# Kernel optimization log

Measured on AMD Instinct MI355X. Metric: run time of the kernel, lower is better.

The kernel has to match this reference:

```python
import jax, jax.numpy as jnp
import numpy as np


def setup_inputs() -> dict:
    key = jax.random.key(0)
    k1, k2, k3, k4 = jax.random.split(key, 4)
    B, D_vis, E, N = 512, 4096, 1024, 512
    vf = jax.random.normal(k1, (B, D_vis), dtype=jnp.float32)
    p_lfs = jax.random.normal(k2, (B, E), dtype=jnp.float32)
    n_lfs = jax.random.normal(k3, (N, E), dtype=jnp.float32)
    W = jax.random.normal(k4, (E, D_vis), dtype=jnp.float32) * (1.0 / np.sqrt(D_vis))
    b = jnp.zeros((E,), dtype=jnp.float32)
    return {"vf": vf, "p_lfs": p_lfs, "n_lfs": n_lfs, "W": W, "b": b}


def _partial_order_sim(hypers, hypos):
    # -||relu(hypers - hypos)||_2 along last dim
    act = jax.nn.relu(hypers - hypos)
    return -jnp.sqrt(jnp.sum(act * act, axis=-1))


def reference(vf, p_lfs, n_lfs, W, b):
    # vf: [B, D_vis], W: [E, D_vis] -> vf_emb: [B, E]
    vf_emb = jnp.einsum("bd,ed->be", vf, W) + b
    # positive scores: [B]
    p_scores = _partial_order_sim(p_lfs, vf_emb)
    # negative scores, batched over B: n_lfs [N,E] vs vf_emb [B,E] -> [B,N]
    n_scores = _partial_order_sim(n_lfs[None, :, :], vf_emb[:, None, :])
    # score_stack: [B, 1+N]
    return jnp.concatenate([p_scores[:, None], n_scores], axis=1)
```

## Files before the change

kernel.cpp:

```cpp
#include <hip/hip_runtime.h>
#include <hip/hip_bf16.h>

constexpr int B = 512;
constexpr int D = 4096;
constexpr int E = 1024;
constexpr int N = 512;
constexpr int KS = 8;
constexpr int KC = D / KS;
constexpr int NSTEP = KC / 32;
constexpr int ES = 8;
constexpr int EC = E / ES;
constexpr int DEPTH = 4;

typedef __attribute__((ext_vector_type(8))) short bf16x8;
typedef __attribute__((ext_vector_type(4))) float f32x4;
typedef float v2f __attribute__((ext_vector_type(2)));

typedef __attribute__((address_space(3))) void lds_void;
typedef const __attribute__((address_space(1))) void gbl_void;

__device__ __forceinline__ unsigned short f2bf(float f) {
    __hip_bfloat16 h = __float2bfloat16(f);
    return *reinterpret_cast<unsigned short*>(&h);
}

__global__ __launch_bounds__(256) void cvt_all(
    const float* __restrict__ vf, const float* __restrict__ W,
    unsigned short* __restrict__ vfB, unsigned short* __restrict__ WB)
{
    const int bid = blockIdx.x;
    const float* src;
    unsigned short* dst;
    int i;
    if (bid < 1024) { src = vf; dst = vfB; i = (bid * 256 + threadIdx.x) * 8; }
    else           { src = W;  dst = WB;  i = ((bid - 1024) * 256 + threadIdx.x) * 8; }
    float4 v0 = *(const float4*)(src + i);
    float4 v1 = *(const float4*)(src + i + 4);
    bf16x8 o;
    o[0] = (short)f2bf(v0.x); o[1] = (short)f2bf(v0.y);
    o[2] = (short)f2bf(v0.z); o[3] = (short)f2bf(v0.w);
    o[4] = (short)f2bf(v1.x); o[5] = (short)f2bf(v1.y);
    o[6] = (short)f2bf(v1.z); o[7] = (short)f2bf(v1.w);
    *(bf16x8*)(dst + i) = o;
}

__global__ __launch_bounds__(64) void gemm_lds(
    const unsigned short* __restrict__ vf,
    const unsigned short* __restrict__ W,
    float* __restrict__ part)
{
    __shared__ unsigned short sA[DEPTH][2048];
    __shared__ unsigned short sB[DEPTH][2048];

    const int L  = threadIdx.x;

    const int id = blockIdx.x + 16 * blockIdx.y + 128 * blockIdx.z;
    const int l  = (id & 7) * 128 + (id >> 3);
    const int ks = l >> 7;
    const int n0 = (l & 15) * 64;
    const int m0 = ((l >> 4) & 7) * 64;

    const int subrow = L >> 2;
    const int qstg = (L & 3) ^ ((L >> 2) & 3) ^ ((L >> 4) & 3);
    const int kbeg = ks * KC;
    const unsigned short* aSrc[4];
    const unsigned short* bSrc[4];
    #pragma unroll
    for (int c = 0; c < 4; ++c) {
        aSrc[c] = vf + (size_t)(m0 + c * 16 + subrow) * D + kbeg + qstg * 8;
        bSrc[c] = W  + (size_t)(n0 + c * 16 + subrow) * D + kbeg + qstg * 8;
    }

    const int r16 = L & 15;
    const int quad = L >> 4;
    const int swz = quad ^ (r16 & 3) ^ ((r16 >> 2) & 3);
    const int aoff = r16 * 64 + swz * 16;

    f32x4 acc[4][4] = {};

    auto issue = [&](int step, int buf) {
        const size_t koff = (size_t)step * 32;
        #pragma unroll
        for (int c = 0; c < 4; ++c) {
            __builtin_amdgcn_global_load_lds(
                (gbl_void*)(aSrc[c] + koff),
                (lds_void*)((char*)&sA[buf][0] + c * 1024), 16, 0, 0);
            __builtin_amdgcn_global_load_lds(
                (gbl_void*)(bSrc[c] + koff),
                (lds_void*)((char*)&sB[buf][0] + c * 1024), 16, 0, 0);
        }
    };

    issue(0, 0);
    issue(1, 1);
    issue(2, 2);
    issue(3, 3);

    #define GSTEP(S, WC, ISS)                                                  \
    {                                                                          \
        const int buf_ = (S) & 3;                                              \
        __builtin_amdgcn_s_waitcnt(WC);                                        \
        bf16x8 af[4], bg[4];                                                   \
        _Pragma("unroll")                                                      \
        for (int i = 0; i < 4; ++i)                                            \
            af[i] = *(const bf16x8*)((const char*)&sA[buf_][0] + i * 1024 + aoff); \
        _Pragma("unroll")                                                      \
        for (int j = 0; j < 4; ++j)                                            \
            bg[j] = *(const bf16x8*)((const char*)&sB[buf_][0] + j * 1024 + aoff); \
        _Pragma("unroll")                                                      \
        for (int i = 0; i < 4; ++i)                                            \
            _Pragma("unroll")                                                  \
            for (int j = 0; j < 4; ++j)                                        \
                acc[i][j] = __builtin_amdgcn_mfma_f32_16x16x32_bf16(           \
                    af[i], bg[j], acc[i][j], 0, 0, 0);                         \
        if (ISS) issue((S) + DEPTH, buf_);                                     \
    }

    #pragma unroll 1
    for (int s = 0; s < NSTEP - DEPTH; ++s)
        GSTEP(s, 0x4F78, true);
    GSTEP(NSTEP - 4, 0x4F78, false);
    GSTEP(NSTEP - 3, 0x4F70, false);
    GSTEP(NSTEP - 2, 0x0F78, false);
    GSTEP(NSTEP - 1, 0x0F70, false);
    #undef GSTEP

    float* po = part + (size_t)ks * B * E;
    #pragma unroll
    for (int j = 0; j < 4; ++j) {
        const int col = n0 + j * 16 + r16;
        #pragma unroll
        for (int i = 0; i < 4; ++i) {
            const int row = m0 + i * 16 + quad * 4;
            #pragma unroll
            for (int r = 0; r < 4; ++r)
                po[(size_t)(row + r) * E + col] = acc[i][j][r];
        }
    }
}

__global__ __launch_bounds__(256) void reduce_emb(
    const float* __restrict__ part, const float* __restrict__ bias,
    float* __restrict__ emb)
{
    const int idx = (blockIdx.x * 256 + threadIdx.x) * 4;
    const int col = idx & (E - 1);
    float4 s = *(const float4*)(bias + col);
    #pragma unroll
    for (int ks = 0; ks < KS; ++ks) {
        float4 p = *(const float4*)(part + (size_t)ks * B * E + idx);
        s.x += p.x; s.y += p.y; s.z += p.z; s.w += p.w;
    }
    *(float4*)(emb + idx) = s;
}

__global__ __launch_bounds__(256, 2) void scores_part(
    const float* __restrict__ emb,
    const float* __restrict__ n_lfs,
    float* __restrict__ pn)
{
    constexpr int LDW = EC + 2;
    __shared__ float eS[64 * LDW];
    __shared__ float nS[64 * LDW];

    const int t  = threadIdx.x;
    const int n0 = blockIdx.x * 64;
    const int b0 = blockIdx.y * 64;
    const int e0 = blockIdx.z * EC;

    {
        const int row = t >> 2;
        const int cb  = (t & 3) * 32;
        const float* ep = emb   + (size_t)(b0 + row) * E + e0 + cb;
        const float* np = n_lfs + (size_t)(n0 + row) * E + e0 + cb;
        float* ed = &eS[row * LDW + cb];
        float* nd = &nS[row * LDW + cb];
        #pragma unroll
        for (int q = 0; q < 8; ++q) {
            float4 v = *(const float4*)(ep + q * 4);
            float4 w = *(const float4*)(np + q * 4);
            *(v2f*)(ed + q * 4)     = (v2f){v.x, v.y};
            *(v2f*)(ed + q * 4 + 2) = (v2f){v.z, v.w};
            *(v2f*)(nd + q * 4)     = (v2f){w.x, w.y};
            *(v2f*)(nd + q * 4 + 2) = (v2f){w.z, w.w};
        }
    }
    __syncthreads();

    const int ty = t >> 4;
    const int tx = t & 15;

    const v2f z = {0.f, 0.f};
    v2f acc[4][4] = {{z,z,z,z},{z,z,z,z},{z,z,z,z},{z,z,z,z}};

    #pragma unroll 4
    for (int e = 0; e < EC; e += 2) {
        v2f a[4], c[4];
        #pragma unroll
        for (int r = 0; r < 4; ++r)
            a[r] = *(const v2f*)&eS[(ty + 16 * r) * LDW + e];
        #pragma unroll
        for (int q = 0; q < 4; ++q)
            c[q] = *(const v2f*)&nS[(tx + 16 * q) * LDW + e];
        #pragma unroll
        for (int r = 0; r < 4; ++r)
            #pragma unroll
            for (int q = 0; q < 4; ++q) {
                v2f d = c[q] - a[r];
                d = __builtin_elementwise_max(d, z);
                acc[r][q] = __builtin_elementwise_fma(d, d, acc[r][q]);
            }
    }

    float* po = pn + (size_t)blockIdx.z * B * N;
    #pragma unroll
    for (int r = 0; r < 4; ++r) {
        const size_t ob = (size_t)(b0 + ty + 16 * r) * N;
        #pragma unroll
        for (int q = 0; q < 4; ++q)
            po[ob + n0 + tx + 16 * q] = acc[r][q].x + acc[r][q].y;
    }
}

__global__ __launch_bounds__(256) void scores_final(
    const float* __restrict__ pn,
    const float* __restrict__ emb,
    const float* __restrict__ p_lfs,
    float* __restrict__ out)
{
    const int t = threadIdx.x;
    if (blockIdx.x < 1024) {
        const int i = blockIdx.x * 256 + t;
        const int b = i >> 9;
        const int n = i & (N - 1);
        float s = 0.f;
        #pragma unroll
        for (int z = 0; z < ES; ++z)
            s += pn[(size_t)z * B * N + i];
        out[(size_t)b * 513 + 1 + n] = -sqrtf(s);
        return;
    }
    const int b0 = (blockIdx.x - 1024) * 32;
    const int r = t >> 3;
    const int g = t & 7;
    const float* pr = p_lfs + (size_t)(b0 + r) * E;
    const float* er = emb   + (size_t)(b0 + r) * E;
    float acc = 0.f;
    for (int e = g * 4; e < E; e += 32) {
        float4 p = *(const float4*)(pr + e);
        float4 v = *(const float4*)(er + e);
        float d;
        d = p.x - v.x; d = fmaxf(d, 0.f); acc = fmaf(d, d, acc);
        d = p.y - v.y; d = fmaxf(d, 0.f); acc = fmaf(d, d, acc);
        d = p.z - v.z; d = fmaxf(d, 0.f); acc = fmaf(d, d, acc);
        d = p.w - v.w; d = fmaxf(d, 0.f); acc = fmaf(d, d, acc);
    }
    #pragma unroll
    for (int off = 4; off; off >>= 1) acc += __shfl_down(acc, off, 8);
    if (g == 0) out[(size_t)(b0 + r) * 513] = -sqrtf(acc);
}

extern "C" void kernel_launch(void* const* d_in, const int* in_sizes, int n_in,
                              void* d_out, int out_size, void* d_ws, size_t ws_size,
                              hipStream_t stream) {
    const float* vf    = (const float*)d_in[0];
    const float* p_lfs = (const float*)d_in[1];
    const float* n_lfs = (const float*)d_in[2];
    const float* W     = (const float*)d_in[3];
    const float* bias  = (const float*)d_in[4];
    float* out = (float*)d_out;

    char* ws = (char*)d_ws;
    float*          pg  = (float*)ws;
    float*          pn  = (float*)ws;
    unsigned short* vfB = (unsigned short*)(ws + ((size_t)16 << 20));
    unsigned short* WB  = (unsigned short*)(ws + ((size_t)20 << 20));
    float*          emb = (float*)(ws + ((size_t)28 << 20));

    cvt_all<<<3072, 256, 0, stream>>>(vf, W, vfB, WB);

    dim3 g1(E / 64, B / 64, KS);
    gemm_lds<<<g1, 64, 0, stream>>>(vfB, WB, pg);

    reduce_emb<<<(B * E) / 1024, 256, 0, stream>>>(pg, bias, emb);

    dim3 g3(N / 64, B / 64, ES);
    scores_part<<<g3, 256, 0, stream>>>(emb, n_lfs, pn);

    scores_final<<<1024 + B / 32, 256, 0, stream>>>(pn, emb, p_lfs, out);
}
```

Baseline: 132.8 us.

## Use fp16 packed math for negative scores, stage GEMM epilogue through LDS

Converts n_lfs and the embedding to fp16 and computes the relu-squared-distance with packed half adds, max and fdot2 into fp32 accumulators. This halves LDS and global traffic in the scores kernel and raises its occupancy hint. The GEMM epilogue now transposes through LDS so partial sums are written as coalesced float4 rows. The positive-score computation is fused into the split-K reduction kernel. Using fp16 for the distance inputs and differences lowers accuracy.

```diff
diff --git a/kernel.cpp b/kernel.cpp
--- a/kernel.cpp
+++ b/kernel.cpp
@@ -14,7 +14,9 @@
 
 typedef __attribute__((ext_vector_type(8))) short bf16x8;
 typedef __attribute__((ext_vector_type(4))) float f32x4;
-typedef float v2f __attribute__((ext_vector_type(2)));
+typedef _Float16 h2 __attribute__((ext_vector_type(2)));
+typedef _Float16 h4 __attribute__((ext_vector_type(4)));
+typedef _Float16 h8 __attribute__((ext_vector_type(8)));
 
 typedef __attribute__((address_space(3))) void lds_void;
 typedef const __attribute__((address_space(1))) void gbl_void;
@@ -24,24 +26,48 @@
     return *reinterpret_cast<unsigned short*>(&h);
 }
 
+#if __has_builtin(__builtin_amdgcn_fdot2)
+__device__ __forceinline__ float fdot2(h2 a, h2 b, float c) {
+    return __builtin_amdgcn_fdot2(a, b, c, false);
+}
+#else
+__device__ __forceinline__ float fdot2(h2 a, h2 b, float c) {
+    return c + (float)a[0] * (float)b[0] + (float)a[1] * (float)b[1];
+}
+#endif
+
 __global__ __launch_bounds__(256) void cvt_all(
     const float* __restrict__ vf, const float* __restrict__ W,
-    unsigned short* __restrict__ vfB, unsigned short* __restrict__ WB)
+    const float* __restrict__ n_lfs,
+    unsigned short* __restrict__ vfB, unsigned short* __restrict__ WB,
+    _Float16* __restrict__ n16)
 {
     const int bid = blockIdx.x;
-    const float* src;
-    unsigned short* dst;
-    int i;
-    if (bid < 1024) { src = vf; dst = vfB; i = (bid * 256 + threadIdx.x) * 8; }
-    else           { src = W;  dst = WB;  i = ((bid - 1024) * 256 + threadIdx.x) * 8; }
-    float4 v0 = *(const float4*)(src + i);
-    float4 v1 = *(const float4*)(src + i + 4);
-    bf16x8 o;
-    o[0] = (short)f2bf(v0.x); o[1] = (short)f2bf(v0.y);
-    o[2] = (short)f2bf(v0.z); o[3] = (short)f2bf(v0.w);
-    o[4] = (short)f2bf(v1.x); o[5] = (short)f2bf(v1.y);
-    o[6] = (short)f2bf(v1.z); o[7] = (short)f2bf(v1.w);
-    *(bf16x8*)(dst + i) = o;
+    if (bid < 3072) {
+        const float* src;
+        unsigned short* dst;
+        int i;
+        if (bid < 1024) { src = vf; dst = vfB; i = (bid * 256 + threadIdx.x) * 8; }
+        else           { src = W;  dst = WB;  i = ((bid - 1024) * 256 + threadIdx.x) * 8; }
+        float4 v0 = *(const float4*)(src + i);
+        float4 v1 = *(const float4*)(src + i + 4);
+        bf16x8 o;
+        o[0] = (short)f2bf(v0.x); o[1] = (short)f2bf(v0.y);
+        o[2] = (short)f2bf(v0.z); o[3] = (short)f2bf(v0.w);
+        o[4] = (short)f2bf(v1.x); o[5] = (short)f2bf(v1.y);
+        o[6] = (short)f2bf(v1.z); o[7] = (short)f2bf(v1.w);
+        *(bf16x8*)(dst + i) = o;
+    } else {
+        const int i = ((bid - 3072) * 256 + threadIdx.x) * 8;
+        float4 v0 = *(const float4*)(n_lfs + i);
+        float4 v1 = *(const float4*)(n_lfs + i + 4);
+        h8 o;
+        o[0] = (_Float16)v0.x; o[1] = (_Float16)v0.y;
+        o[2] = (_Float16)v0.z; o[3] = (_Float16)v0.w;
+        o[4] = (_Float16)v1.x; o[5] = (_Float16)v1.y;
+        o[6] = (_Float16)v1.z; o[7] = (_Float16)v1.w;
+        *(h8*)(n16 + i) = o;
+    }
 }
 
 __global__ __launch_bounds__(64) void gemm_lds(
@@ -49,8 +75,7 @@
     const unsigned short* __restrict__ W,
     float* __restrict__ part)
 {
-    __shared__ unsigned short sA[DEPTH][2048];
-    __shared__ unsigned short sB[DEPTH][2048];
+    __shared__ __align__(16) char smem[32768];
 
     const int L  = threadIdx.x;
 
@@ -84,10 +109,10 @@
         for (int c = 0; c < 4; ++c) {
             __builtin_amdgcn_global_load_lds(
                 (gbl_void*)(aSrc[c] + koff),
-                (lds_void*)((char*)&sA[buf][0] + c * 1024), 16, 0, 0);
+                (lds_void*)(smem + buf * 4096 + c * 1024), 16, 0, 0);
             __builtin_amdgcn_global_load_lds(
                 (gbl_void*)(bSrc[c] + koff),
-                (lds_void*)((char*)&sB[buf][0] + c * 1024), 16, 0, 0);
+                (lds_void*)(smem + 16384 + buf * 4096 + c * 1024), 16, 0, 0);
         }
     };
 
@@ -103,10 +128,10 @@
         bf16x8 af[4], bg[4];                                                   \
         _Pragma("unroll")                                                      \
         for (int i = 0; i < 4; ++i)                                            \
-            af[i] = *(const bf16x8*)((const char*)&sA[buf_][0] + i * 1024 + aoff); \
+            af[i] = *(const bf16x8*)(smem + buf_ * 4096 + i * 1024 + aoff);    \
         _Pragma("unroll")                                                      \
         for (int j = 0; j < 4; ++j)                                            \
-            bg[j] = *(const bf16x8*)((const char*)&sB[buf_][0] + j * 1024 + aoff); \
+            bg[j] = *(const bf16x8*)(smem + 16384 + buf_ * 4096 + j * 1024 + aoff); \
         _Pragma("unroll")                                                      \
         for (int i = 0; i < 4; ++i)                                            \
             _Pragma("unroll")                                                  \
@@ -125,43 +150,69 @@
     GSTEP(NSTEP - 1, 0x0F70, false);
     #undef GSTEP
 
-    float* po = part + (size_t)ks * B * E;
-    #pragma unroll
-    for (int j = 0; j < 4; ++j) {
-        const int col = n0 + j * 16 + r16;
-        #pragma unroll
-        for (int i = 0; i < 4; ++i) {
-            const int row = m0 + i * 16 + quad * 4;
+    float* ct = (float*)smem;
+    #pragma unroll
+    for (int i = 0; i < 4; ++i)
+        #pragma unroll
+        for (int j = 0; j < 4; ++j)
             #pragma unroll
             for (int r = 0; r < 4; ++r)
-                po[(size_t)(row + r) * E + col] = acc[i][j][r];
-        }
+                ct[(i * 16 + quad * 4 + r) * 69 + (j * 16 + r16)] = acc[i][j][r];
+    __builtin_amdgcn_s_waitcnt(0xC07F);
+    __builtin_amdgcn_sched_barrier(0);
+    float* po = part + (size_t)ks * B * E + (size_t)(m0 + L) * E + n0;
+    const float* crow = ct + L * 69;
+    #pragma unroll
+    for (int c4 = 0; c4 < 16; ++c4) {
+        f32x4 v;
+        v[0] = crow[c4 * 4];     v[1] = crow[c4 * 4 + 1];
+        v[2] = crow[c4 * 4 + 2]; v[3] = crow[c4 * 4 + 3];
+        *(f32x4*)(po + c4 * 4) = v;
     }
 }
 
 __global__ __launch_bounds__(256) void reduce_emb(
     const float* __restrict__ part, const float* __restrict__ bias,
-    float* __restrict__ emb)
-{
-    const int idx = (blockIdx.x * 256 + threadIdx.x) * 4;
-    const int col = idx & (E - 1);
-    float4 s = *(const float4*)(bias + col);
+    const float* __restrict__ p_lfs,
+    _Float16* __restrict__ emb16, float* __restrict__ out)
+{
+    const int b = blockIdx.x;
+    const int e = threadIdx.x * 4;
+    const size_t base = (size_t)b * E + e;
+    float4 s = *(const float4*)(bias + e);
     #pragma unroll
     for (int ks = 0; ks < KS; ++ks) {
-        float4 p = *(const float4*)(part + (size_t)ks * B * E + idx);
+        float4 p = *(const float4*)(part + (size_t)ks * B * E + base);
         s.x += p.x; s.y += p.y; s.z += p.z; s.w += p.w;
     }
-    *(float4*)(emb + idx) = s;
-}
-
-__global__ __launch_bounds__(256, 2) void scores_part(
-    const float* __restrict__ emb,
-    const float* __restrict__ n_lfs,
+    h4 o;
+    o[0] = (_Float16)s.x; o[1] = (_Float16)s.y;
+    o[2] = (_Float16)s.z; o[3] = (_Float16)s.w;
+    *(h4*)(emb16 + base) = o;
+
+    const float4 pl = *(const float4*)(p_lfs + base);
+    float d, a = 0.f;
+    d = pl.x - s.x; d = fmaxf(d, 0.f); a = fmaf(d, d, a);
+    d = pl.y - s.y; d = fmaxf(d, 0.f); a = fmaf(d, d, a);
+    d = pl.z - s.z; d = fmaxf(d, 0.f); a = fmaf(d, d, a);
+    d = pl.w - s.w; d = fmaxf(d, 0.f); a = fmaf(d, d, a);
+    #pragma unroll
+    for (int off = 32; off; off >>= 1) a += __shfl_down(a, off, 64);
+    __shared__ float red[4];
+    if ((threadIdx.x & 63) == 0) red[threadIdx.x >> 6] = a;
+    __syncthreads();
+    if (threadIdx.x == 0)
+        out[(size_t)b * 513] = -sqrtf(red[0] + red[1] + red[2] + red[3]);
+}
+
+__global__ __launch_bounds__(256, 4) void scores_part(
+    const _Float16* __restrict__ emb16,
+    const _Float16* __restrict__ n16,
     float* __restrict__ pn)
 {
-    constexpr int LDW = EC + 2;
-    __shared__ float eS[64 * LDW];
-    __shared__ float nS[64 * LDW];
+    constexpr int LDH = EC + 8;
+    __shared__ _Float16 eS[64 * LDH];
+    __shared__ _Float16 nS[64 * LDH];
 
     const int t  = threadIdx.x;
     const int n0 = blockIdx.x * 64;
@@ -171,18 +222,16 @@
     {
         const int row = t >> 2;
         const int cb  = (t & 3) * 32;
-        const float* ep = emb   + (size_t)(b0 + row) * E + e0 + cb;
-        const float* np = n_lfs + (size_t)(n0 + row) * E + e0 + cb;
-        float* ed = &eS[row * LDW + cb];
-        float* nd = &nS[row * LDW + cb];
-        #pragma unroll
-        for (int q = 0; q < 8; ++q) {
-            float4 v = *(const float4*)(ep + q * 4);
-            float4 w = *(const float4*)(np + q * 4);
-            *(v2f*)(ed + q * 4)     = (v2f){v.x, v.y};
-            *(v2f*)(ed + q * 4 + 2) = (v2f){v.z, v.w};
-            *(v2f*)(nd + q * 4)     = (v2f){w.x, w.y};
-            *(v2f*)(nd + q * 4 + 2) = (v2f){w.z, w.w};
+        const _Float16* ep = emb16 + (size_t)(b0 + row) * E + e0 + cb;
+        const _Float16* np = n16   + (size_t)(n0 + row) * E + e0 + cb;
+        _Float16* ed = &eS[row * LDH + cb];
+        _Float16* nd = &nS[row * LDH + cb];
+        #pragma unroll
+        for (int q = 0; q < 4; ++q) {
+            h8 v = *(const h8*)(ep + q * 8);
+            h8 w = *(const h8*)(np + q * 8);
+            *(h8*)(ed + q * 8) = -v;
+            *(h8*)(nd + q * 8) = w;
         }
     }
     __syncthreads();
@@ -190,25 +239,28 @@
     const int ty = t >> 4;
     const int tx = t & 15;
 
-    const v2f z = {0.f, 0.f};
-    v2f acc[4][4] = {{z,z,z,z},{z,z,z,z},{z,z,z,z},{z,z,z,z}};
-
-    #pragma unroll 4
-    for (int e = 0; e < EC; e += 2) {
-        v2f a[4], c[4];
+    float acc[4][4] = {};
+    const h4 z4 = {};
+
+    #pragma unroll 2
+    for (int e = 0; e < EC; e += 4) {
+        h4 a[4], c[4];
         #pragma unroll
         for (int r = 0; r < 4; ++r)
-            a[r] = *(const v2f*)&eS[(ty + 16 * r) * LDW + e];
+            a[r] = *(const h4*)&eS[(ty + 16 * r) * LDH + e];
         #pragma unroll
         for (int q = 0; q < 4; ++q)
-            c[q] = *(const v2f*)&nS[(tx + 16 * q) * LDW + e];
+            c[q] = *(const h4*)&nS[(tx + 16 * q) * LDH + e];
         #pragma unroll
         for (int r = 0; r < 4; ++r)
             #pragma unroll
             for (int q = 0; q < 4; ++q) {
-                v2f d = c[q] - a[r];
-                d = __builtin_elementwise_max(d, z);
-                acc[r][q] = __builtin_elementwise_fma(d, d, acc[r][q]);
+                h4 d = c[q] + a[r];
+                d = __builtin_elementwise_max(d, z4);
+                h2 dl = __builtin_shufflevector(d, d, 0, 1);
+                h2 dh = __builtin_shufflevector(d, d, 2, 3);
+                acc[r][q] = fdot2(dl, dl, acc[r][q]);
+                acc[r][q] = fdot2(dh, dh, acc[r][q]);
             }
     }
 
@@ -218,46 +270,22 @@
         const size_t ob = (size_t)(b0 + ty + 16 * r) * N;
         #pragma unroll
         for (int q = 0; q < 4; ++q)
-            po[ob + n0 + tx + 16 * q] = acc[r][q].x + acc[r][q].y;
+            po[ob + n0 + tx + 16 * q] = acc[r][q];
     }
 }
 
 __global__ __launch_bounds__(256) void scores_final(
     const float* __restrict__ pn,
-    const float* __restrict__ emb,
-    const float* __restrict__ p_lfs,
     float* __restrict__ out)
 {
-    const int t = threadIdx.x;
-    if (blockIdx.x < 1024) {
-        const int i = blockIdx.x * 256 + t;
-        const int b = i >> 9;
-        const int n = i & (N - 1);
-        float s = 0.f;
-        #pragma unroll
-        for (int z = 0; z < ES; ++z)
-            s += pn[(size_t)z * B * N + i];
-        out[(size_t)b * 513 + 1 + n] = -sqrtf(s);
-        return;
-    }
-    const int b0 = (blockIdx.x - 1024) * 32;
-    const int r = t >> 3;
-    const int g = t & 7;
-    const float* pr = p_lfs + (size_t)(b0 + r) * E;
-    const float* er = emb   + (size_t)(b0 + r) * E;
-    float acc = 0.f;
-    for (int e = g * 4; e < E; e += 32) {
-        float4 p = *(const float4*)(pr + e);
-        float4 v = *(const float4*)(er + e);
-        float d;
-        d = p.x - v.x; d = fmaxf(d, 0.f); acc = fmaf(d, d, acc);
-        d = p.y - v.y; d = fmaxf(d, 0.f); acc = fmaf(d, d, acc);
-        d = p.z - v.z; d = fmaxf(d, 0.f); acc = fmaf(d, d, acc);
-        d = p.w - v.w; d = fmaxf(d, 0.f); acc = fmaf(d, d, acc);
-    }
-    #pragma unroll
-    for (int off = 4; off; off >>= 1) acc += __shfl_down(acc, off, 8);
-    if (g == 0) out[(size_t)(b0 + r) * 513] = -sqrtf(acc);
+    const int i = blockIdx.x * 256 + threadIdx.x;
+    const int b = i >> 9;
+    const int n = i & (N - 1);
+    float s = 0.f;
+    #pragma unroll
+    for (int z = 0; z < ES; ++z)
+        s += pn[(size_t)z * B * N + i];
+    out[(size_t)b * 513 + 1 + n] = -sqrtf(s);
 }
 
 extern "C" void kernel_launch(void* const* d_in, const int* in_sizes, int n_in,
@@ -271,21 +299,22 @@
     float* out = (float*)d_out;
 
     char* ws = (char*)d_ws;
-    float*          pg  = (float*)ws;
-    float*          pn  = (float*)ws;
-    unsigned short* vfB = (unsigned short*)(ws + ((size_t)16 << 20));
-    unsigned short* WB  = (unsigned short*)(ws + ((size_t)20 << 20));
-    float*          emb = (float*)(ws + ((size_t)28 << 20));
-
-    cvt_all<<<3072, 256, 0, stream>>>(vf, W, vfB, WB);
+    float*          pg    = (float*)ws;
+    float*          pn    = (float*)ws;
+    unsigned short* vfB   = (unsigned short*)(ws + ((size_t)16 << 20));
+    unsigned short* WB    = (unsigned short*)(ws + ((size_t)20 << 20));
+    _Float16*       emb16 = (_Float16*)(ws + ((size_t)28 << 20));
+    _Float16*       n16   = (_Float16*)(ws + ((size_t)29 << 20));
+
+    cvt_all<<<3328, 256, 0, stream>>>(vf, W, n_lfs, vfB, WB, n16);
 
     dim3 g1(E / 64, B / 64, KS);
     gemm_lds<<<g1, 64, 0, stream>>>(vfB, WB, pg);
 
-    reduce_emb<<<(B * E) / 1024, 256, 0, stream>>>(pg, bias, emb);
+    reduce_emb<<<B, 256, 0, stream>>>(pg, bias, p_lfs, emb16, out);
 
     dim3 g3(N / 64, B / 64, ES);
-    scores_part<<<g3, 256, 0, stream>>>(emb, n_lfs, pn);
-
-    scores_final<<<1024 + B / 32, 256, 0, stream>>>(pn, emb, p_lfs, out);
-}
+    scores_part<<<g3, 256, 0, stream>>>(emb16, n16, pn);
+
+    scores_final<<<(B * N) / 256, 256, 0, stream>>>(pn, out);
+}
```

Measured after the change: 120.7 us. 1.1x faster.
